# Optimization experiments

Measured on AMD Instinct MI355X. Metric: run time of the kernel, lower is better.

The kernel has to match this reference:

```python
import jax, jax.numpy as jnp
import numpy as np

PATCH_SIZE = 2  # init arg patch_size


def setup_inputs() -> dict:
    key = jax.random.key(0)
    k1, k2, k3, k4, k5 = jax.random.split(key, 5)
    b, H, W, d = 8, 32, 32, 256
    n_obj = 15
    patches = jax.random.normal(k1, (b, H, W, d), jnp.float32)
    embs = jax.random.normal(k2, (b, n_obj, 256), jnp.float32)
    locations = jax.random.randint(k3, (b, n_obj, 4), 0, 32, jnp.int32)
    Wp = jax.random.normal(k4, (256, 256), jnp.float32) * 0.05
    We = jax.random.normal(k5, (256, 256), jnp.float32) * 0.05
    return {"patches": patches, "embs": embs, "locations": locations, "Wp": Wp, "We": We}


def _build_masks(locations, b, H, W):
    # patching(): floor starts / ceil ends to multiples of PATCH_SIZE
    starts = locations[..., :2] - locations[..., :2] % PATCH_SIZE
    ends = locations[..., 2:] + (PATCH_SIZE - locations[..., 2:] % PATCH_SIZE)
    locs = jnp.concatenate([starts, ends], axis=-1)          # [b, n_obj, 4]
    img = jnp.broadcast_to(jnp.array([0, 0, H, W], locs.dtype), (b, 1, 4))
    locs = jnp.concatenate([locs, img], axis=1)              # [b, n, 4]
    rows = jnp.arange(H)[:, None]                             # [H,1]
    cols = jnp.arange(W)[None, :]                             # [1,W]
    y0 = locs[..., 0, None, None]; x0 = locs[..., 1, None, None]
    y1 = locs[..., 2, None, None]; x1 = locs[..., 3, None, None]
    # vectorized box rasterization (replaces torch slice-assign scatter loops)
    m = (rows >= y0) & (rows < y1) & (cols >= x0) & (cols < x1)  # [b,n,H,W]
    return m.reshape(b, locs.shape[1], H * W)                 # [b,n,HW]


def reference(patches, embs, locations, Wp, We):
    b, H, W, d = patches.shape
    # append mean embedding (torch: cat([embs, embs.mean(dim=1, keepdim=True)]))
    embs = jnp.concatenate([embs, embs.mean(axis=1, keepdims=True)], axis=1)  # [b,n,e]
    masks = _build_masks(locations, b, H, W)                  # [b,n,HW] bool
    mf = masks.astype(patches.dtype)
    # InjectionBlock (assumed minimal): project patches, inject masked emb
    proj = jnp.einsum('bpd,do->bpo', patches.reshape(b, H * W, d), Wp)  # [b,HW,o]
    inj = jnp.einsum('bne,eo->bno', embs, We)                 # [b,n,o]
    p = proj[:, None] + mf[..., None] * inj[:, :, None, :]    # [b,n,HW,o]
    # masked mean pooling over the n mask channels
    out = (p * mf[..., None]).sum(axis=1) / mf.sum(axis=1)[..., None]  # [b,HW,o]
    return out
```

## Files before the change

### kernel.cpp

```cpp
#include <hip/hip_runtime.h>

typedef short short8 __attribute__((ext_vector_type(8)));
typedef float f32x4 __attribute__((ext_vector_type(4)));

static __device__ __forceinline__ unsigned short f2bf(float f) {
    unsigned u = __builtin_bit_cast(unsigned, f);
    u += 0x7FFFu + ((u >> 16) & 1u);
    return (unsigned short)(u >> 16);
}
static __device__ __forceinline__ float bf2f(unsigned short h) {
    unsigned u = ((unsigned)h) << 16;
    return __builtin_bit_cast(float, u);
}

#define OFF_INJT (128 * 1024)

__global__ __launch_bounds__(256)
void prep_kernel(const float* __restrict__ embs,
                 const float* __restrict__ Wp,
                 const float* __restrict__ We,
                 unsigned short* __restrict__ Btg,
                 unsigned short* __restrict__ injT) {
    __shared__ float sh[64 * 65];
    __shared__ unsigned short Ebf[16 * 256];

    const int bid = blockIdx.x, t = threadIdx.x;

    if (bid < 16) {
        const int kt = (bid >> 2) * 64, n0 = (bid & 3) * 64;
        #pragma unroll
        for (int it = 0; it < 16; ++it) {
            int u = t + it * 256;
            int kl = u >> 6, nl = u & 63;
            sh[kl * 65 + nl] = Wp[(kt + kl) * 256 + n0 + nl];
        }
        __syncthreads();
        #pragma unroll
        for (int it = 0; it < 4; ++it) {
            int v = t + it * 256;
            int nl = v >> 4, kg = v & 15;
            ushort4 o;
            o.x = f2bf(sh[(kg * 4 + 0) * 65 + nl]);
            o.y = f2bf(sh[(kg * 4 + 1) * 65 + nl]);
            o.z = f2bf(sh[(kg * 4 + 2) * 65 + nl]);
            o.w = f2bf(sh[(kg * 4 + 3) * 65 + nl]);
            int ks = (kt >> 5) + (kg >> 3);
            int n16 = (n0 >> 4) + (nl >> 4);
            int idx = ks * 8192 + n16 * 512 + (nl & 15) * 32 + ((kg >> 1) & 3) * 8 + (kg & 1) * 4;
            *reinterpret_cast<ushort4*>(&Btg[idx]) = o;
        }
    } else {
        const int ib = bid - 16;
        const int b = ib >> 2, oq = ib & 3;

        if (t < 128) {
            const int c0 = t * 2;
            #pragma unroll
            for (int r = 0; r < 15; ++r) {
                float2 v = *reinterpret_cast<const float2*>(embs + (size_t)(b * 15 + r) * 256 + c0);
                unsigned pk = (unsigned)f2bf(v.x) | ((unsigned)f2bf(v.y) << 16);
                *reinterpret_cast<unsigned*>(reinterpret_cast<char*>(Ebf)
                    + r * 512 + ((c0 * 2) ^ ((r & 7) << 4))) = pk;
            }
        }
        __syncthreads();
        if (t < 128) {
            const int c0 = t * 2;
            float s0 = 0.f, s1 = 0.f;
            #pragma unroll
            for (int r = 0; r < 15; ++r) {
                unsigned pk = *reinterpret_cast<const unsigned*>(reinterpret_cast<char*>(Ebf)
                    + r * 512 + ((c0 * 2) ^ ((r & 7) << 4)));
                s0 += bf2f((unsigned short)(pk & 0xffffu));
                s1 += bf2f((unsigned short)(pk >> 16));
            }
            unsigned pk = (unsigned)f2bf(s0 * (1.0f / 15.0f))
                        | ((unsigned)f2bf(s1 * (1.0f / 15.0f)) << 16);
            *reinterpret_cast<unsigned*>(reinterpret_cast<char*>(Ebf)
                + 15 * 512 + ((c0 * 2) ^ ((7) << 4))) = pk;
        }
        __syncthreads();

        const int wv = t >> 6, lane = t & 63, lhi = lane >> 4, llo = lane & 15;
        const int oc = oq * 64 + wv * 16 + llo;

        f32x4 acc = (f32x4){0.f, 0.f, 0.f, 0.f};
        #pragma unroll
        for (int ks = 0; ks < 8; ++ks) {
            const short8 afr = *reinterpret_cast<const short8*>(
                reinterpret_cast<const char*>(Ebf)
                + llo * 512 + ((ks * 64 + lhi * 16) ^ ((llo & 7) << 4)));
            short8 bfr;
            #pragma unroll
            for (int r = 0; r < 8; ++r)
                bfr[r] = (short)f2bf(We[(size_t)(ks * 32 + lhi * 8 + r) * 256 + oc]);
            acc = __builtin_amdgcn_mfma_f32_16x16x32_bf16(afr, bfr, acc, 0, 0, 0);
        }
        ushort4 o4;
        o4.x = f2bf(acc[0]); o4.y = f2bf(acc[1]);
        o4.z = f2bf(acc[2]); o4.w = f2bf(acc[3]);
        unsigned short* dst = injT + (size_t)b * 8192 + (oq * 4 + wv) * 512 + llo * 32;
        *reinterpret_cast<ushort4*>(dst + lhi * 4) = o4;
        ushort4 z = {0, 0, 0, 0};
        *reinterpret_cast<ushort4*>(dst + 16 + lhi * 4) = z;
    }
}

__global__ __launch_bounds__(256)
void fused_kernel(const float* __restrict__ patches,
                  const int* __restrict__ locations,
                  const unsigned short* __restrict__ Btg,
                  const unsigned short* __restrict__ injT,
                  float* __restrict__ out) {
    __shared__ unsigned maskL[16];
    __shared__ float rcL[16];

    const int bid = blockIdx.x, t = threadIdx.x;
    const int b = bid >> 6, p0 = (bid & 63) * 16;
    const int wv = t >> 6, lane = t & 63, lhi = lane >> 4, llo = lane & 15;

    if (t < 16) {
        int p = p0 + t;
        int h = p >> 5, w = p & 31;
        const int* loc = locations + b * 60;
        unsigned m = 1u << 15;
        #pragma unroll
        for (int nb = 0; nb < 15; ++nb) {
            int y0 = loc[nb * 4 + 0] & ~1;
            int x0 = loc[nb * 4 + 1] & ~1;
            int y1 = (loc[nb * 4 + 2] & ~1) + 2;
            int x1 = (loc[nb * 4 + 3] & ~1) + 2;
            if (h >= y0 && h < y1 && w >= x0 && w < x1) m |= 1u << nb;
        }
        maskL[t] = m;
        rcL[t] = 1.0f / (float)__popc(m);
    }

    const float* arow = patches + (size_t)(b * 1024 + p0 + llo) * 256;
    float4 a0[8], a1[8];
    #pragma unroll
    for (int ks = 0; ks < 8; ++ks) {
        a0[ks] = *reinterpret_cast<const float4*>(arow + ks * 32 + lhi * 8);
        a1[ks] = *reinterpret_cast<const float4*>(arow + ks * 32 + lhi * 8 + 4);
    }
    short8 af[8];
    #pragma unroll
    for (int ks = 0; ks < 8; ++ks) {
        short8 a;
        a[0] = (short)f2bf(a0[ks].x); a[1] = (short)f2bf(a0[ks].y);
        a[2] = (short)f2bf(a0[ks].z); a[3] = (short)f2bf(a0[ks].w);
        a[4] = (short)f2bf(a1[ks].x); a[5] = (short)f2bf(a1[ks].y);
        a[6] = (short)f2bf(a1[ks].z); a[7] = (short)f2bf(a1[ks].w);
        af[ks] = a;
    }

    f32x4 acc[4];
    #pragma unroll
    for (int nt = 0; nt < 4; ++nt) acc[nt] = (f32x4){0.f, 0.f, 0.f, 0.f};
    #pragma unroll
    for (int ks = 0; ks < 8; ++ks) {
        #pragma unroll
        for (int nt = 0; nt < 4; ++nt) {
            const short8 bf = *reinterpret_cast<const short8*>(
                Btg + ks * 8192 + (wv * 4 + nt) * 512 + llo * 32 + lhi * 8);
            acc[nt] = __builtin_amdgcn_mfma_f32_16x16x32_bf16(af[ks], bf, acc[nt], 0, 0, 0);
        }
    }

    __syncthreads();

    unsigned m = maskL[llo];
    short8 mfrag;
    #pragma unroll
    for (int r = 0; r < 8; ++r) {
        int k = lhi * 8 + r;
        mfrag[r] = (k < 16 && ((m >> k) & 1u)) ? (short)0x3F80 : (short)0;
    }
    f32x4 accE[4];
    #pragma unroll
    for (int nt = 0; nt < 4; ++nt) {
        const short8 jf = *reinterpret_cast<const short8*>(
            injT + b * 8192 + (wv * 4 + nt) * 512 + llo * 32 + lhi * 8);
        accE[nt] = __builtin_amdgcn_mfma_f32_16x16x32_bf16(
            mfrag, jf, (f32x4){0.f, 0.f, 0.f, 0.f}, 0, 0, 0);
    }

    float rc[4];
    #pragma unroll
    for (int j = 0; j < 4; ++j) rc[j] = rcL[lhi * 4 + j];

    float* ob = out + ((size_t)b * 1024 + p0) * 256;
    #pragma unroll
    for (int nt = 0; nt < 4; ++nt)
        #pragma unroll
        for (int j = 0; j < 4; ++j)
            ob[(lhi * 4 + j) * 256 + wv * 64 + nt * 16 + llo] = acc[nt][j] + rc[j] * accE[nt][j];
}

extern "C" void kernel_launch(void* const* d_in, const int* in_sizes, int n_in,
                              void* d_out, int out_size, void* d_ws, size_t ws_size,
                              hipStream_t stream) {
    const float* patches = (const float*)d_in[0];
    const float* embs    = (const float*)d_in[1];
    const int*   locs    = (const int*)d_in[2];
    const float* Wp      = (const float*)d_in[3];
    const float* We      = (const float*)d_in[4];
    float* out = (float*)d_out;

    unsigned short* Btg  = (unsigned short*)d_ws;
    unsigned short* injT = (unsigned short*)((char*)d_ws + OFF_INJT);

    prep_kernel<<<48, 256, 0, stream>>>(embs, Wp, We, Btg, injT);
    fused_kernel<<<512, 256, 0, stream>>>(patches, locs, Btg, injT, out);
}
```

Measured before the change: 19.59 us.

## Split output columns across 8 waves, drop shared mask sync, fold reciprocal into mask

The fused kernel now launches 512 threads per block, so 8 waves each own 32 output columns instead of 4 waves owning 64. This halves per-wave MFMA and accumulator work but makes every wave reload and reconvert the same patch rows. Each lane now computes the box mask itself, which removes the shared-memory mask table and the __syncthreads. The 1/count reciprocal is folded into the bf16 mask fragment, which adds rounding of the weight to bf16. Float-to-bf16 conversion now uses the packed v_cvt_pk_bf16_f32 instruction.

Measured after the change: 25.00 us. 27.6% more time.

```diff
diff --git a/kernel.cpp b/kernel.cpp
--- a/kernel.cpp
+++ b/kernel.cpp
@@ -11,6 +11,11 @@
 static __device__ __forceinline__ float bf2f(unsigned short h) {
     unsigned u = ((unsigned)h) << 16;
     return __builtin_bit_cast(float, u);
+}
+static __device__ __forceinline__ unsigned cvtpk_bf16(float lo, float hi) {
+    unsigned r;
+    asm("v_cvt_pk_bf16_f32 %0, %1, %2" : "=v"(r) : "v"(lo), "v"(hi));
+    return r;
 }
 
 #define OFF_INJT (128 * 1024)
@@ -106,95 +111,80 @@
     }
 }
 
-__global__ __launch_bounds__(256)
+__global__ __launch_bounds__(512, 4)
 void fused_kernel(const float* __restrict__ patches,
                   const int* __restrict__ locations,
                   const unsigned short* __restrict__ Btg,
                   const unsigned short* __restrict__ injT,
                   float* __restrict__ out) {
-    __shared__ unsigned maskL[16];
-    __shared__ float rcL[16];
-
     const int bid = blockIdx.x, t = threadIdx.x;
     const int b = bid >> 6, p0 = (bid & 63) * 16;
     const int wv = t >> 6, lane = t & 63, lhi = lane >> 4, llo = lane & 15;
 
-    if (t < 16) {
-        int p = p0 + t;
-        int h = p >> 5, w = p & 31;
-        const int* loc = locations + b * 60;
-        unsigned m = 1u << 15;
-        #pragma unroll
-        for (int nb = 0; nb < 15; ++nb) {
-            int y0 = loc[nb * 4 + 0] & ~1;
-            int x0 = loc[nb * 4 + 1] & ~1;
-            int y1 = (loc[nb * 4 + 2] & ~1) + 2;
-            int x1 = (loc[nb * 4 + 3] & ~1) + 2;
-            if (h >= y0 && h < y1 && w >= x0 && w < x1) m |= 1u << nb;
-        }
-        maskL[t] = m;
-        rcL[t] = 1.0f / (float)__popc(m);
-    }
-
-    const float* arow = patches + (size_t)(b * 1024 + p0 + llo) * 256;
-    float4 a0[8], a1[8];
-    #pragma unroll
-    for (int ks = 0; ks < 8; ++ks) {
-        a0[ks] = *reinterpret_cast<const float4*>(arow + ks * 32 + lhi * 8);
-        a1[ks] = *reinterpret_cast<const float4*>(arow + ks * 32 + lhi * 8 + 4);
-    }
-    short8 af[8];
-    #pragma unroll
-    for (int ks = 0; ks < 8; ++ks) {
-        short8 a;
-        a[0] = (short)f2bf(a0[ks].x); a[1] = (short)f2bf(a0[ks].y);
-        a[2] = (short)f2bf(a0[ks].z); a[3] = (short)f2bf(a0[ks].w);
-        a[4] = (short)f2bf(a1[ks].x); a[5] = (short)f2bf(a1[ks].y);
-        a[6] = (short)f2bf(a1[ks].z); a[7] = (short)f2bf(a1[ks].w);
-        af[ks] = a;
-    }
-
-    f32x4 acc[4];
-    #pragma unroll
-    for (int nt = 0; nt < 4; ++nt) acc[nt] = (f32x4){0.f, 0.f, 0.f, 0.f};
-    #pragma unroll
-    for (int ks = 0; ks < 8; ++ks) {
-        #pragma unroll
-        for (int nt = 0; nt < 4; ++nt) {
-            const short8 bf = *reinterpret_cast<const short8*>(
-                Btg + ks * 8192 + (wv * 4 + nt) * 512 + llo * 32 + lhi * 8);
-            acc[nt] = __builtin_amdgcn_mfma_f32_16x16x32_bf16(af[ks], bf, acc[nt], 0, 0, 0);
-        }
-    }
-
-    __syncthreads();
-
-    unsigned m = maskL[llo];
+    const int p = p0 + llo, h = p >> 5, w = p & 31;
+    const int* loc = locations + b * 60;
+    unsigned m = 1u << 15;
+    #pragma unroll
+    for (int nb = 0; nb < 15; ++nb) {
+        int y0 = loc[nb * 4 + 0] & ~1;
+        int x0 = loc[nb * 4 + 1] & ~1;
+        int y1 = (loc[nb * 4 + 2] & ~1) + 2;
+        int x1 = (loc[nb * 4 + 3] & ~1) + 2;
+        if (h >= y0 && h < y1 && w >= x0 && w < x1) m |= 1u << nb;
+    }
+    const unsigned short rcb = f2bf(1.0f / (float)__popc(m));
     short8 mfrag;
     #pragma unroll
     for (int r = 0; r < 8; ++r) {
         int k = lhi * 8 + r;
-        mfrag[r] = (k < 16 && ((m >> k) & 1u)) ? (short)0x3F80 : (short)0;
-    }
-    f32x4 accE[4];
-    #pragma unroll
-    for (int nt = 0; nt < 4; ++nt) {
-        const short8 jf = *reinterpret_cast<const short8*>(
-            injT + b * 8192 + (wv * 4 + nt) * 512 + llo * 32 + lhi * 8);
-        accE[nt] = __builtin_amdgcn_mfma_f32_16x16x32_bf16(
-            mfrag, jf, (f32x4){0.f, 0.f, 0.f, 0.f}, 0, 0, 0);
-    }
-
-    float rc[4];
-    #pragma unroll
-    for (int j = 0; j < 4; ++j) rc[j] = rcL[lhi * 4 + j];
+        mfrag[r] = (k < 16 && ((m >> k) & 1u)) ? (short)rcb : (short)0;
+    }
+
+    f32x4 accE[2];
+    {
+        const short8 jf0 = *reinterpret_cast<const short8*>(
+            injT + (size_t)b * 8192 + (wv * 2 + 0) * 512 + llo * 32 + lhi * 8);
+        const short8 jf1 = *reinterpret_cast<const short8*>(
+            injT + (size_t)b * 8192 + (wv * 2 + 1) * 512 + llo * 32 + lhi * 8);
+        accE[0] = __builtin_amdgcn_mfma_f32_16x16x32_bf16(
+            mfrag, jf0, (f32x4){0.f, 0.f, 0.f, 0.f}, 0, 0, 0);
+        accE[1] = __builtin_amdgcn_mfma_f32_16x16x32_bf16(
+            mfrag, jf1, (f32x4){0.f, 0.f, 0.f, 0.f}, 0, 0, 0);
+    }
+
+    const float* arow = patches + (size_t)(b * 1024 + p0 + llo) * 256;
+    short8 af[8];
+    #pragma unroll
+    for (int ks = 0; ks < 8; ++ks) {
+        float4 f0 = *reinterpret_cast<const float4*>(arow + ks * 32 + lhi * 8);
+        float4 f1 = *reinterpret_cast<const float4*>(arow + ks * 32 + lhi * 8 + 4);
+        union { short8 s; unsigned u[4]; } A;
+        A.u[0] = cvtpk_bf16(f0.x, f0.y);
+        A.u[1] = cvtpk_bf16(f0.z, f0.w);
+        A.u[2] = cvtpk_bf16(f1.x, f1.y);
+        A.u[3] = cvtpk_bf16(f1.z, f1.w);
+        af[ks] = A.s;
+    }
+
+    f32x4 acc[2];
+    acc[0] = (f32x4){0.f, 0.f, 0.f, 0.f};
+    acc[1] = (f32x4){0.f, 0.f, 0.f, 0.f};
+    #pragma unroll
+    for (int ks = 0; ks < 8; ++ks) {
+        #pragma unroll
+        for (int nt = 0; nt < 2; ++nt) {
+            const short8 bf = *reinterpret_cast<const short8*>(
+                Btg + ks * 8192 + (wv * 2 + nt) * 512 + llo * 32 + lhi * 8);
+            acc[nt] = __builtin_amdgcn_mfma_f32_16x16x32_bf16(af[ks], bf, acc[nt], 0, 0, 0);
+        }
+    }
 
     float* ob = out + ((size_t)b * 1024 + p0) * 256;
     #pragma unroll
-    for (int nt = 0; nt < 4; ++nt)
+    for (int nt = 0; nt < 2; ++nt)
         #pragma unroll
         for (int j = 0; j < 4; ++j)
-            ob[(lhi * 4 + j) * 256 + wv * 64 + nt * 16 + llo] = acc[nt][j] + rc[j] * accE[nt][j];
+            ob[(lhi * 4 + j) * 256 + (wv * 2 + nt) * 16 + llo] = acc[nt][j] + accE[nt][j];
 }
 
 extern "C" void kernel_launch(void* const* d_in, const int* in_sizes, int n_in,
@@ -211,5 +201,5 @@
     unsigned short* injT = (unsigned short*)((char*)d_ws + OFF_INJT);
 
     prep_kernel<<<48, 256, 0, stream>>>(embs, Wp, We, Btg, injT);
-    fused_kernel<<<512, 256, 0, stream>>>(patches, locs, Btg, injT, out);
-}
+    fused_kernel<<<512, 512, 0, stream>>>(patches, locs, Btg, injT, out);
+}
```
